# Performance work log

Measured on AMD Instinct MI355X. Metric: run time of the kernel, lower is better.

## Reference

```python
import jax, jax.numpy as jnp
import numpy as np

B, T, D, H = 4, 4096, 1024, 16
DH = D // H
NB = T // 2 + 1  # rfft bins


def setup_inputs() -> dict:
    key = jax.random.key(0)
    ks = jax.random.split(key, 6)
    x = jax.random.normal(ks[0], (B, T, D), dtype=jnp.float32)
    # torch nn.Linear params: weight [out, in], bias [out]
    W_qkv = jax.random.normal(ks[1], (3 * D, D), dtype=jnp.float32) * 0.02
    b_qkv = jnp.zeros((3 * D,), dtype=jnp.float32)
    W_o = jax.random.normal(ks[2], (D, D), dtype=jnp.float32) * 0.02
    b_o = jnp.zeros((D,), dtype=jnp.float32)
    # per-head per-bin spectral filters (smart-init-like small values)
    log_gain = jax.random.normal(ks[3], (H, NB), dtype=jnp.float32) * 0.05
    phase = jax.random.normal(ks[4], (H, NB), dtype=jnp.float32) * 0.01
    return {"x": x, "W_qkv": W_qkv, "b_qkv": b_qkv, "W_o": W_o,
            "b_o": b_o, "log_gain": log_gain, "phase": phase}


def reference(x, W_qkv, b_qkv, W_o, b_o, log_gain, phase):
    # qkv projection; only v is used on the spectral path (q,k discarded)
    qkv = jnp.einsum('btd,ed->bte', x, W_qkv) + b_qkv  # [B,T,3D]
    v = qkv[..., 2 * D:]                               # [B,T,D]
    v = v.reshape(B, T, H, DH).transpose(0, 2, 1, 3)   # [B,H,T,DH]
    # rFFT along the token dim
    v_f = jnp.fft.rfft(v.astype(jnp.float32), axis=2)  # [B,H,NB,DH] complex
    # per-head per-bin complex filter: polar(exp(log_gain), phase)
    mag = jnp.exp(log_gain)
    comp = jax.lax.complex(mag * jnp.cos(phase), mag * jnp.sin(phase))  # [H,NB]
    v_f = v_f * comp[None, :, :, None]
    y_h = jnp.fft.irfft(v_f, n=T, axis=2)              # [B,H,T,DH]
    y = y_h.transpose(0, 2, 1, 3).reshape(B, T, D)     # [B,T,D]
    y = jnp.einsum('btd,ed->bte', y, W_o) + b_o
    return x + y
```

## Files before the change

kernel.cpp:

```cpp
#include <hip/hip_runtime.h>
#include <hip/hip_bf16.h>
#include <math.h>

#define B_BATCH 4
#define T_LEN   4096
#define D_DIM   1024
#define H_HEADS 16
#define NB_BINS 2049
#define M_ROWS  (B_BATCH * T_LEN)

typedef __attribute__((ext_vector_type(8))) short short8;
typedef __attribute__((ext_vector_type(8))) unsigned short u16x8;
typedef __attribute__((ext_vector_type(4))) float f32x4;

__device__ __forceinline__ ushort f2bf(float f) {
    unsigned b = __float_as_uint(f);
    unsigned r = (b + 0x7fffu + ((b >> 16) & 1u)) >> 16;
    return (ushort)r;
}
__device__ __forceinline__ float bf2f(ushort u) {
    return __uint_as_float(((unsigned)u) << 16);
}
__device__ __forceinline__ u16x8 pack8(const float4& a, const float4& b) {
    u16x8 o;
    o[0] = f2bf(a.x); o[1] = f2bf(a.y); o[2] = f2bf(a.z); o[3] = f2bf(a.w);
    o[4] = f2bf(b.x); o[5] = f2bf(b.y); o[6] = f2bf(b.z); o[7] = f2bf(b.w);
    return o;
}

__global__ void cvt_weights(const float* __restrict__ wv, const float* __restrict__ wo,
                            ushort* __restrict__ wvb, ushort* __restrict__ wob, int n4) {
    int i = blockIdx.x * 256 + threadIdx.x;
    const float* src = (i < n4) ? wv : wo;
    ushort* dst = (i < n4) ? wvb : wob;
    int j = (i < n4) ? i : (i - n4);
    float4 v = ((const float4*)src)[j];
    ushort4 o;
    o.x = f2bf(v.x); o.y = f2bf(v.y); o.z = f2bf(v.z); o.w = f2bf(v.w);
    ((ushort4*)dst)[j] = o;
}

__device__ __forceinline__ int drev16(int i) {
    return ((i & 15) << 8) | (i & 0xF0) | (i >> 8);
}

__global__ void prep_tables(const float* __restrict__ lg, const float* __restrict__ ph,
                            float2* __restrict__ Cdr, float2* __restrict__ tw) {
    int idx = blockIdx.x * 256 + threadIdx.x;
    if (idx < 4096) {
        double th = -2.0 * 3.14159265358979323846 * (double)idx / 4096.0;
        tw[idx] = make_float2((float)cos(th), (float)sin(th));
    }
    if (idx >= H_HEADS * 4096) return;
    int h = idx >> 12, i = idx & 4095;
    int f = drev16(i);
    int fc = (f <= 2048) ? f : (4096 - f);
    float sgn = (f <= 2048) ? 1.f : -1.f;
    float m = expf(lg[h * NB_BINS + fc]) * (1.0f / 4096.0f);
    float p = ph[h * NB_BINS + fc];
    float re = m * __cosf(p), im = sgn * m * __sinf(p);
    if (fc == 0 || fc == 2048) im = 0.f;
    Cdr[idx] = make_float2(re, im);
}

template<bool RESID, bool BIASROW, bool BF32>
__global__ __launch_bounds__(512, 1) void gemm256(const ushort* __restrict__ A,
        const void* __restrict__ Bv, const float* __restrict__ bias,
        const float* __restrict__ resid, void* __restrict__ Cout,
        int M, int N, int K) {
    __shared__ ushort lds[65536];
    const int tid  = threadIdx.x;
    const int lane = tid & 63;
    const int wid  = tid >> 6;
    const int wr   = wid >> 2, wc = wid & 3;
    const int fr   = lane & 15;
    const int nbn  = N >> 8;
    int bid = (int)blockIdx.x;
    bid = (bid & 7) * ((int)gridDim.x >> 3) + (bid >> 3);
    int bm, bn;
    if (BF32) { const int nbm = M >> 8; bm = bid % nbm; bn = bid / nbm; }
    else      { bm = bid / nbn; bn = bid % nbn; }
    const int row0 = bm << 8, col0 = bn << 8;
    const int NT = K >> 6;

    const ushort* Bu = (const ushort*)Bv;
    const float*  Bf = (const float*)Bv;

    f32x4 acc[8][4];
#pragma unroll
    for (int i = 0; i < 8; i++)
#pragma unroll
        for (int j = 0; j < 4; j++) acc[i][j] = (f32x4){0.f, 0.f, 0.f, 0.f};

    auto stageA = [&](int t, int s) {
        int base = (((t & 1) << 1) + s) << 13;
        int k0 = (t << 6) + (s << 5);
#pragma unroll
        for (int i = 0; i < 2; i++) {
            int r = (wid << 5) + (i << 4) + (lane >> 2);
            int c = ((lane & 3) ^ ((lane >> 3) & 3)) << 3;
            const ushort* g = A + (size_t)(row0 + r) * (size_t)K + (size_t)(k0 + c);
            __builtin_amdgcn_global_load_lds(
                (const __attribute__((address_space(1))) void*)g,
                (__attribute__((address_space(3))) void*)&lds[base + (((wid << 1) + i) << 9)],
                16, 0, 0);
        }
    };
    auto stageB = [&](int t, int s) {
        int base = 32768 + ((((t & 1) << 1) + s) << 13);
        int k0 = (t << 6) + (s << 5);
#pragma unroll
        for (int i = 0; i < 2; i++) {
            int r = (wid << 5) + (i << 4) + (lane >> 2);
            int c = ((lane & 3) ^ ((lane >> 3) & 3)) << 3;
            const ushort* g = Bu + (size_t)(col0 + r) * (size_t)K + (size_t)(k0 + c);
            __builtin_amdgcn_global_load_lds(
                (const __attribute__((address_space(1))) void*)g,
                (__attribute__((address_space(3))) void*)&lds[base + (((wid << 1) + i) << 9)],
                16, 0, 0);
        }
    };
    auto issueB = [&](int t, int s, float4 bR[2][2]) {
#pragma unroll
        for (int i = 0; i < 2; i++) {
            int row = (wid << 5) + (i << 4) + (lane >> 2);
            int cc  = lane & 3;
            const float* g = Bf + (size_t)(col0 + row) * (size_t)K
                           + (size_t)((t << 6) + (s << 5) + (cc << 3));
            bR[i][0] = *(const float4*)g;
            bR[i][1] = *(const float4*)(g + 4);
        }
    };
    auto writeB = [&](int t, int s, float4 bR[2][2]) {
        int base = 32768 + ((((t & 1) << 1) + s) << 13);
#pragma unroll
        for (int i = 0; i < 2; i++) {
            int row = (wid << 5) + (i << 4) + (lane >> 2);
            int cc  = lane & 3;
            int slot = cc ^ ((row >> 1) & 3);
            *(u16x8*)&lds[base + (row << 5) + (slot << 3)] = pack8(bR[i][0], bR[i][1]);
        }
    };
    auto rdfrag = [&](int base, int row) -> short8 {
        int g = (((lane >> 4) ^ ((row >> 1) & 3)) << 3);
        return *(const short8*)&lds[base + (row << 5) + g];
    };

    stageA(0, 0); stageA(0, 1);
    if (BF32) {
        float4 bR0[2][2], bR1[2][2];
        issueB(0, 0, bR0); issueB(0, 1, bR1);
        writeB(0, 0, bR0); writeB(0, 1, bR1);
    } else {
        stageB(0, 0); stageB(0, 1);
    }
    __syncthreads();

    for (int t = 0; t < NT; ++t) {
        const int d = t & 1;
        const bool pre = (t + 1) < NT;
        float4 bR[2][2];
        if (pre) {
            stageA(t + 1, 0); stageA(t + 1, 1);
            if (BF32) issueB(t + 1, 0, bR);
            else { stageB(t + 1, 0); stageB(t + 1, 1); }
        }
        {
            const int ab = (((d << 1) + 0) << 13);
            const int bb = 32768 + (((d << 1) + 0) << 13);
            short8 bFr[4], aF[4];
#pragma unroll
            for (int ni = 0; ni < 4; ni++) bFr[ni] = rdfrag(bb, (wc << 6) + (ni << 4) + fr);
#pragma unroll
            for (int mh = 0; mh < 2; mh++) {
#pragma unroll
                for (int mi = 0; mi < 4; mi++)
                    aF[mi] = rdfrag(ab, (wr << 7) + (mh << 6) + (mi << 4) + fr);
#pragma unroll
                for (int mi = 0; mi < 4; mi++)
#pragma unroll
                    for (int ni = 0; ni < 4; ni++)
                        acc[(mh << 2) + mi][ni] = __builtin_amdgcn_mfma_f32_16x16x32_bf16(
                            aF[mi], bFr[ni], acc[(mh << 2) + mi][ni], 0, 0, 0);
            }
        }
        if (BF32 && pre) { writeB(t + 1, 0, bR); issueB(t + 1, 1, bR); }
        {
            const int ab = (((d << 1) + 1) << 13);
            const int bb = 32768 + (((d << 1) + 1) << 13);
            short8 bFr[4], aF[4];
#pragma unroll
            for (int ni = 0; ni < 4; ni++) bFr[ni] = rdfrag(bb, (wc << 6) + (ni << 4) + fr);
#pragma unroll
            for (int mh = 0; mh < 2; mh++) {
#pragma unroll
                for (int mi = 0; mi < 4; mi++)
                    aF[mi] = rdfrag(ab, (wr << 7) + (mh << 6) + (mi << 4) + fr);
#pragma unroll
                for (int mi = 0; mi < 4; mi++)
#pragma unroll
                    for (int ni = 0; ni < 4; ni++)
                        acc[(mh << 2) + mi][ni] = __builtin_amdgcn_mfma_f32_16x16x32_bf16(
                            aF[mi], bFr[ni], acc[(mh << 2) + mi][ni], 0, 0, 0);
            }
        }
        if (BF32 && pre) writeB(t + 1, 1, bR);
        __syncthreads();
    }

    const int crow = (lane >> 4) << 2;
#pragma unroll
    for (int mi = 0; mi < 8; mi++) {
#pragma unroll
        for (int ni = 0; ni < 4; ni++) {
            int row = row0 + (wr << 7) + (mi << 4) + crow;
            int col = col0 + (wc << 6) + (ni << 4) + fr;
            float bcol = BIASROW ? 0.f : bias[col];
#pragma unroll
            for (int j = 0; j < 4; j++) {
                float v = acc[mi][ni][j] + (BIASROW ? bias[row + j] : bcol);
                size_t off = (size_t)(row + j) * N + col;
                if (RESID) ((float*)Cout)[off] = resid[off] + v;
                else       ((ushort*)Cout)[off] = f2bf(v);
            }
        }
    }
}

__device__ __forceinline__ float2 cadd(float2 a, float2 b){ return make_float2(a.x+b.x, a.y+b.y); }
__device__ __forceinline__ float2 csub(float2 a, float2 b){ return make_float2(a.x-b.x, a.y-b.y); }
__device__ __forceinline__ float2 jmulp(float2 z){ return make_float2(-z.y, z.x); }
__device__ __forceinline__ float2 cmul(float2 a, float2 b){
    return make_float2(fmaf(a.x,b.x,-a.y*b.y), fmaf(a.x,b.y, a.y*b.x)); }
__device__ __forceinline__ float2 cmulc(float2 a, float2 b){
    return make_float2(fmaf(a.x,b.x, a.y*b.y), fmaf(a.y,b.x,-a.x*b.y)); }

template<int INV>
__device__ __forceinline__ void bf4(float2& a, float2& b, float2& c, float2& d) {
    float2 acp = cadd(a,c), acm = csub(a,c);
    float2 bdp = cadd(b,d), bdm = csub(b,d);
    float2 jb  = jmulp(bdm);
    a = cadd(acp, bdp);
    c = csub(acp, bdp);
    if (INV) { b = cadd(acm, jb); d = csub(acm, jb); }
    else     { b = csub(acm, jb); d = cadd(acm, jb); }
}

#define C16_1 0.9238795325112867f
#define S16_1 0.3826834323650898f
#define R16_2 0.7071067811865476f

template<int INV>
__device__ __forceinline__ void dft16(float2 v[16]) {
    const float sg = INV ? 1.f : -1.f;
    bf4<INV>(v[0], v[4], v[8],  v[12]);
    bf4<INV>(v[1], v[5], v[9],  v[13]);
    bf4<INV>(v[2], v[6], v[10], v[14]);
    bf4<INV>(v[3], v[7], v[11], v[15]);
    const float2 w1 = make_float2( C16_1, sg*S16_1);
    const float2 w2 = make_float2( R16_2, sg*R16_2);
    const float2 w3 = make_float2( S16_1, sg*C16_1);
    const float2 w6 = make_float2(-R16_2, sg*R16_2);
    const float2 w9 = make_float2(-C16_1,-sg*S16_1);
    v[5]  = cmul(v[5],  w1);
    v[6]  = cmul(v[6],  w2);
    v[7]  = cmul(v[7],  w3);
    v[9]  = cmul(v[9],  w2);
    v[10] = INV ? jmulp(v[10]) : make_float2(v[10].y, -v[10].x);
    v[11] = cmul(v[11], w6);
    v[13] = cmul(v[13], w3);
    v[14] = cmul(v[14], w6);
    v[15] = cmul(v[15], w9);
    bf4<INV>(v[0],  v[1],  v[2],  v[3]);
    bf4<INV>(v[4],  v[5],  v[6],  v[7]);
    bf4<INV>(v[8],  v[9],  v[10], v[11]);
    bf4<INV>(v[12], v[13], v[14], v[15]);
}

__host__ __device__ constexpr int oidx(int r) { return ((r & 3) << 2) | (r >> 2); }

template<int INV>
__device__ __forceinline__ void dft16p(float2 v[16]) {
    const float sg = INV ? 1.f : -1.f;
    bf4<INV>(v[oidx(0)], v[oidx(4)], v[oidx(8)],  v[oidx(12)]);
    bf4<INV>(v[oidx(1)], v[oidx(5)], v[oidx(9)],  v[oidx(13)]);
    bf4<INV>(v[oidx(2)], v[oidx(6)], v[oidx(10)], v[oidx(14)]);
    bf4<INV>(v[oidx(3)], v[oidx(7)], v[oidx(11)], v[oidx(15)]);
    const float2 w1 = make_float2( C16_1, sg*S16_1);
    const float2 w2 = make_float2( R16_2, sg*R16_2);
    const float2 w3 = make_float2( S16_1, sg*C16_1);
    const float2 w6 = make_float2(-R16_2, sg*R16_2);
    const float2 w9 = make_float2(-C16_1,-sg*S16_1);
    v[oidx(5)]  = cmul(v[oidx(5)],  w1);
    v[oidx(6)]  = cmul(v[oidx(6)],  w2);
    v[oidx(7)]  = cmul(v[oidx(7)],  w3);
    v[oidx(9)]  = cmul(v[oidx(9)],  w2);
    v[oidx(10)] = INV ? jmulp(v[oidx(10)]) : make_float2(v[oidx(10)].y, -v[oidx(10)].x);
    v[oidx(11)] = cmul(v[oidx(11)], w6);
    v[oidx(13)] = cmul(v[oidx(13)], w3);
    v[oidx(14)] = cmul(v[oidx(14)], w6);
    v[oidx(15)] = cmul(v[oidx(15)], w9);
    bf4<INV>(v[oidx(0)],  v[oidx(1)],  v[oidx(2)],  v[oidx(3)]);
    bf4<INV>(v[oidx(4)],  v[oidx(5)],  v[oidx(6)],  v[oidx(7)]);
    bf4<INV>(v[oidx(8)],  v[oidx(9)],  v[oidx(10)], v[oidx(11)]);
    bf4<INV>(v[oidx(12)], v[oidx(13)], v[oidx(14)], v[oidx(15)]);
}

__device__ __forceinline__ int phz(int t) { return t ^ (((t >> 4) ^ (t >> 8)) & 15); }

template<typename F>
__device__ __forceinline__ void tw_powers(float2 w1, F&& apply) {
    apply(1, w1);
    float2 w2 = cmul(w1, w1);   apply(2, w2);
    float2 w3 = cmul(w2, w1);   apply(3, w3);
    float2 w4 = cmul(w2, w2);   apply(4, w4);
    float2 w5 = cmul(w4, w1);   apply(5, w5);
    float2 w6 = cmul(w4, w2);   apply(6, w6);
    float2 w7 = cmul(w4, w3);   apply(7, w7);
    float2 w8 = cmul(w4, w4);   apply(8, w8);
    apply(9,  cmul(w8, w1));
    apply(10, cmul(w8, w2));
    apply(11, cmul(w8, w3));
    apply(12, cmul(w8, w4));
    apply(13, cmul(w8, w5));
    apply(14, cmul(w8, w6));
    apply(15, cmul(w8, w7));
}

__global__ __launch_bounds__(256) void fft16_filter(const ushort* __restrict__ VT,
                                                    ushort* __restrict__ yT,
                                                    const float2* __restrict__ tw,
                                                    const float2* __restrict__ Cdr) {
    __shared__ float2 X[2][4096];
    const int tid = threadIdx.x;
    const int b   = blockIdx.x >> 8;
    const int qb  = blockIdx.x & 255;
    const int d0  = qb << 2;
    const int h   = qb >> 4;

    float2 v[2][16];
#pragma unroll
    for (int p = 0; p < 2; p++) {
        const ushort* sRe = VT + (size_t)(d0 + 2 * p) * M_ROWS + b * T_LEN;
        const ushort* sIm = VT + (size_t)(d0 + 2 * p + 1) * M_ROWS + b * T_LEN;
#pragma unroll
        for (int j = 0; j < 16; j++)
            v[p][j] = make_float2(bf2f(sRe[tid + (j << 8)]), bf2f(sIm[tid + (j << 8)]));
    }

    dft16<0>(v[0]);
    dft16<0>(v[1]);
    {
        float2 w1 = tw[tid];
        tw_powers(w1, [&](int r, float2 w) {
            v[0][oidx(r)] = cmul(v[0][oidx(r)], w);
            v[1][oidx(r)] = cmul(v[1][oidx(r)], w);
        });
    }
#pragma unroll
    for (int r = 0; r < 16; r++) {
        int a = phz(tid + (r << 8));
        X[0][a] = v[0][oidx(r)];
        X[1][a] = v[1][oidx(r)];
    }
    __syncthreads();

    const int p2 = tid & 15, g2 = tid >> 4;
    const int base2 = (g2 << 8) + p2;
#pragma unroll
    for (int j = 0; j < 16; j++) {
        int a = phz(base2 + (j << 4));
        v[0][j] = X[0][a];
        v[1][j] = X[1][a];
    }
    dft16<0>(v[0]);
    dft16<0>(v[1]);
#pragma unroll
    for (int r = 1; r < 16; r++) {
        float2 w = tw[(p2 * r) << 4];
        v[0][oidx(r)] = cmul(v[0][oidx(r)], w);
        v[1][oidx(r)] = cmul(v[1][oidx(r)], w);
    }
#pragma unroll
    for (int r = 0; r < 16; r++) {
        int a = phz(base2 + (r << 4));
        X[0][a] = v[0][oidx(r)];
        X[1][a] = v[1][oidx(r)];
    }
    __syncthreads();

    const int base3 = tid << 4;
#pragma unroll
    for (int j = 0; j < 16; j++) {
        int a = phz(base3 + j);
        v[0][j] = X[0][a];
        v[1][j] = X[1][a];
    }
    dft16<0>(v[0]);
    dft16<0>(v[1]);
    const float2* Ch = Cdr + (h << 12) + base3;
#pragma unroll
    for (int r = 0; r < 16; r++) {
        float2 c = Ch[r];
        v[0][oidx(r)] = cmul(v[0][oidx(r)], c);
        v[1][oidx(r)] = cmul(v[1][oidx(r)], c);
    }
    dft16p<1>(v[0]);
    dft16p<1>(v[1]);
#pragma unroll
    for (int r = 0; r < 16; r++) {
        int a = phz(base3 + r);
        X[0][a] = v[0][r];
        X[1][a] = v[1][r];
    }
    __syncthreads();

#pragma unroll
    for (int j = 0; j < 16; j++) {
        int a = phz(base2 + (j << 4));
        v[0][j] = X[0][a];
        v[1][j] = X[1][a];
    }
#pragma unroll
    for (int j = 1; j < 16; j++) {
        float2 w = tw[(p2 * j) << 4];
        v[0][j] = cmulc(v[0][j], w);
        v[1][j] = cmulc(v[1][j], w);
    }
    dft16<1>(v[0]);
    dft16<1>(v[1]);
#pragma unroll
    for (int r = 0; r < 16; r++) {
        int a = phz(base2 + (r << 4));
        X[0][a] = v[0][oidx(r)];
        X[1][a] = v[1][oidx(r)];
    }
    __syncthreads();

#pragma unroll
    for (int j = 0; j < 16; j++) {
        int a = phz(tid + (j << 8));
        v[0][j] = X[0][a];
        v[1][j] = X[1][a];
    }
    {
        float2 w1 = tw[tid];
        tw_powers(w1, [&](int r, float2 w) {
            v[0][r] = cmulc(v[0][r], w);
            v[1][r] = cmulc(v[1][r], w);
        });
    }
    dft16<1>(v[0]);
    dft16<1>(v[1]);
#pragma unroll
    for (int p = 0; p < 2; p++) {
        ushort* dRe = yT + (size_t)(d0 + 2 * p) * M_ROWS + b * T_LEN;
        ushort* dIm = yT + (size_t)(d0 + 2 * p + 1) * M_ROWS + b * T_LEN;
#pragma unroll
        for (int r = 0; r < 16; r++) {
            float2 val = v[p][oidx(r)];
            dRe[tid + (r << 8)] = f2bf(val.x);
            dIm[tid + (r << 8)] = f2bf(val.y);
        }
    }
}

__global__ __launch_bounds__(256) void transpose_yT(const ushort* __restrict__ src,
                                                    ushort* __restrict__ dst) {
    __shared__ ushort tile[4096];
    const int tid = threadIdx.x;
    const int bm = blockIdx.x & 255;
    const int bd = blockIdx.x >> 8;
    const int m0 = bm << 6, d0 = bd << 6;
#pragma unroll
    for (int i = 0; i < 2; i++) {
        int vn = tid + (i << 8);
        int r  = vn >> 3;
        int c8 = (vn & 7) << 3;
        u16x8 val = *(const u16x8*)&src[(size_t)(d0 + r) * M_ROWS + m0 + c8];
#pragma unroll
        for (int q = 0; q < 8; q++)
            tile[(r << 6) | ((c8 + q) ^ r)] = (ushort)val[q];
    }
    __syncthreads();
    const int dc = tid & 63;
    const int wb = tid >> 6;
#pragma unroll
    for (int i = 0; i < 16; i++) {
        int mr = wb + (i << 2);
        dst[(size_t)(m0 + mr) * D_DIM + d0 + dc] = tile[(dc << 6) | (mr ^ dc)];
    }
}

extern "C" void kernel_launch(void* const* d_in, const int* in_sizes, int n_in,
                              void* d_out, int out_size, void* d_ws, size_t ws_size,
                              hipStream_t stream) {
    const float* x    = (const float*)d_in[0];
    const float* Wqkv = (const float*)d_in[1];
    const float* bqkv = (const float*)d_in[2];
    const float* Wo   = (const float*)d_in[3];
    const float* bo   = (const float*)d_in[4];
    const float* lg   = (const float*)d_in[5];
    const float* ph   = (const float*)d_in[6];

    char* ws = (char*)d_ws;
    ushort* ynat = (ushort*)ws;
    ushort* Wvb = (ushort*)(ws + 33554432);
    ushort* Wob = (ushort*)(ws + 35651584);
    float2* tw  = (float2*)(ws + 37748736);
    float2* Cdr = (float2*)(ws + 37781504);

    ushort* VT   = (ushort*)d_out;
    ushort* yT   = (ushort*)((char*)d_out + 33554432);
    float*  out  = (float*)d_out;

    prep_tables<<<(H_HEADS * 4096) / 256, 256, 0, stream>>>(lg, ph, Cdr, tw);
    cvt_weights<<<2 * (1048576 / 4) / 256, 256, 0, stream>>>(
        Wqkv + 2048 * 1024, Wo, Wvb, Wob, 1048576 / 4);

    gemm256<false, true, true><<<(D_DIM / 256) * (M_ROWS / 256), 512, 0, stream>>>(
        Wvb, (const void*)x, bqkv + 2 * D_DIM, nullptr, (void*)VT, D_DIM, M_ROWS, D_DIM);

    fft16_filter<<<B_BATCH * (D_DIM / 4), 256, 0, stream>>>(VT, yT, tw, Cdr);

    transpose_yT<<<(M_ROWS / 64) * (D_DIM / 64), 256, 0, stream>>>(yT, ynat);

    gemm256<true, false, false><<<(M_ROWS / 256) * (D_DIM / 256), 512, 0, stream>>>(
        ynat, (const void*)Wob, bo, x, (void*)out, M_ROWS, D_DIM, D_DIM);
}
```

Before: 150.2 us.

## Fuse yT transpose into output GEMM A-tile loading

Removes the separate transpose kernel. The output GEMM now reads the d-major yT buffer directly, loading through registers and scattering into the swizzled LDS layout. This saves a full 32 MB read and write pass plus one launch. The cost is that the A operand no longer uses async global_load_lds, and the transposed LDS writes are 16 scalar ushort stores per thread, which may add LDS bank conflicts and register pressure.

```diff
diff --git a/kernel.cpp b/kernel.cpp
--- a/kernel.cpp
+++ b/kernel.cpp
@@ -63,7 +63,7 @@
     Cdr[idx] = make_float2(re, im);
 }
 
-template<bool RESID, bool BIASROW, bool BF32>
+template<bool RESID, bool BIASROW, bool BF32, bool ATR>
 __global__ __launch_bounds__(512, 1) void gemm256(const ushort* __restrict__ A,
         const void* __restrict__ Bv, const float* __restrict__ bias,
         const float* __restrict__ resid, void* __restrict__ Cout,
@@ -106,6 +106,30 @@
                 16, 0, 0);
         }
     };
+    auto issueA_tr = [&](int t, int s, u16x8 aR[2]) {
+        int dl = tid & 31;
+        int m0 = (tid >> 5) << 4;
+        const ushort* g = A + (size_t)((t << 6) + (s << 5) + dl) * (size_t)M
+                        + (size_t)(row0 + m0);
+        aR[0] = *(const u16x8*)g;
+        aR[1] = *(const u16x8*)(g + 8);
+    };
+    auto writeA_tr = [&](int t, int s, u16x8 aR[2]) {
+        int base = (((t & 1) << 1) + s) << 13;
+        int dl = tid & 31;
+        int m0 = (tid >> 5) << 4;
+        int ch = dl >> 3, d7 = dl & 7;
+#pragma unroll
+        for (int j = 0; j < 8; j++) {
+            int m = m0 + j;
+            lds[base + (m << 5) + ((ch ^ ((m >> 1) & 3)) << 3) + d7] = aR[0][j];
+        }
+#pragma unroll
+        for (int j = 0; j < 8; j++) {
+            int m = m0 + 8 + j;
+            lds[base + (m << 5) + ((ch ^ ((m >> 1) & 3)) << 3) + d7] = aR[1][j];
+        }
+    };
     auto stageB = [&](int t, int s) {
         int base = 32768 + ((((t & 1) << 1) + s) << 13);
         int k0 = (t << 6) + (s << 5);
@@ -146,7 +170,13 @@
         return *(const short8*)&lds[base + (row << 5) + g];
     };
 
-    stageA(0, 0); stageA(0, 1);
+    if (ATR) {
+        u16x8 aR0[2], aR1[2];
+        issueA_tr(0, 0, aR0); issueA_tr(0, 1, aR1);
+        writeA_tr(0, 0, aR0); writeA_tr(0, 1, aR1);
+    } else {
+        stageA(0, 0); stageA(0, 1);
+    }
     if (BF32) {
         float4 bR0[2][2], bR1[2][2];
         issueB(0, 0, bR0); issueB(0, 1, bR1);
@@ -160,8 +190,10 @@
         const int d = t & 1;
         const bool pre = (t + 1) < NT;
         float4 bR[2][2];
+        u16x8 aR[2];
         if (pre) {
-            stageA(t + 1, 0); stageA(t + 1, 1);
+            if (ATR) issueA_tr(t + 1, 0, aR);
+            else { stageA(t + 1, 0); stageA(t + 1, 1); }
             if (BF32) issueB(t + 1, 0, bR);
             else { stageB(t + 1, 0); stageB(t + 1, 1); }
         }
@@ -184,7 +216,10 @@
                             aF[mi], bFr[ni], acc[(mh << 2) + mi][ni], 0, 0, 0);
             }
         }
-        if (BF32 && pre) { writeB(t + 1, 0, bR); issueB(t + 1, 1, bR); }
+        if (pre) {
+            if (ATR) { writeA_tr(t + 1, 0, aR); issueA_tr(t + 1, 1, aR); }
+            if (BF32) { writeB(t + 1, 0, bR); issueB(t + 1, 1, bR); }
+        }
         {
             const int ab = (((d << 1) + 1) << 13);
             const int bb = 32768 + (((d << 1) + 1) << 13);
@@ -204,7 +239,10 @@
                             aF[mi], bFr[ni], acc[(mh << 2) + mi][ni], 0, 0, 0);
             }
         }
-        if (BF32 && pre) writeB(t + 1, 1, bR);
+        if (pre) {
+            if (ATR) writeA_tr(t + 1, 1, aR);
+            if (BF32) writeB(t + 1, 1, bR);
+        }
         __syncthreads();
     }
 
@@ -465,33 +503,6 @@
     }
 }
 
-__global__ __launch_bounds__(256) void transpose_yT(const ushort* __restrict__ src,
-                                                    ushort* __restrict__ dst) {
-    __shared__ ushort tile[4096];
-    const int tid = threadIdx.x;
-    const int bm = blockIdx.x & 255;
-    const int bd = blockIdx.x >> 8;
-    const int m0 = bm << 6, d0 = bd << 6;
-#pragma unroll
-    for (int i = 0; i < 2; i++) {
-        int vn = tid + (i << 8);
-        int r  = vn >> 3;
-        int c8 = (vn & 7) << 3;
-        u16x8 val = *(const u16x8*)&src[(size_t)(d0 + r) * M_ROWS + m0 + c8];
-#pragma unroll
-        for (int q = 0; q < 8; q++)
-            tile[(r << 6) | ((c8 + q) ^ r)] = (ushort)val[q];
-    }
-    __syncthreads();
-    const int dc = tid & 63;
-    const int wb = tid >> 6;
-#pragma unroll
-    for (int i = 0; i < 16; i++) {
-        int mr = wb + (i << 2);
-        dst[(size_t)(m0 + mr) * D_DIM + d0 + dc] = tile[(dc << 6) | (mr ^ dc)];
-    }
-}
-
 extern "C" void kernel_launch(void* const* d_in, const int* in_sizes, int n_in,
                               void* d_out, int out_size, void* d_ws, size_t ws_size,
                               hipStream_t stream) {
@@ -504,27 +515,24 @@
     const float* ph   = (const float*)d_in[6];
 
     char* ws = (char*)d_ws;
-    ushort* ynat = (ushort*)ws;
+    ushort* yT  = (ushort*)ws;
     ushort* Wvb = (ushort*)(ws + 33554432);
     ushort* Wob = (ushort*)(ws + 35651584);
     float2* tw  = (float2*)(ws + 37748736);
     float2* Cdr = (float2*)(ws + 37781504);
 
-    ushort* VT   = (ushort*)d_out;
-    ushort* yT   = (ushort*)((char*)d_out + 33554432);
-    float*  out  = (float*)d_out;
+    ushort* VT  = (ushort*)d_out;
+    float*  out = (float*)d_out;
 
     prep_tables<<<(H_HEADS * 4096) / 256, 256, 0, stream>>>(lg, ph, Cdr, tw);
     cvt_weights<<<2 * (1048576 / 4) / 256, 256, 0, stream>>>(
         Wqkv + 2048 * 1024, Wo, Wvb, Wob, 1048576 / 4);
 
-    gemm256<false, true, true><<<(D_DIM / 256) * (M_ROWS / 256), 512, 0, stream>>>(
+    gemm256<false, true, true, false><<<(D_DIM / 256) * (M_ROWS / 256), 512, 0, stream>>>(
         Wvb, (const void*)x, bqkv + 2 * D_DIM, nullptr, (void*)VT, D_DIM, M_ROWS, D_DIM);
 
     fft16_filter<<<B_BATCH * (D_DIM / 4), 256, 0, stream>>>(VT, yT, tw, Cdr);
 
-    transpose_yT<<<(M_ROWS / 64) * (D_DIM / 64), 256, 0, stream>>>(yT, ynat);
-
-    gemm256<true, false, false><<<(M_ROWS / 256) * (D_DIM / 256), 512, 0, stream>>>(
-        ynat, (const void*)Wob, bo, x, (void*)out, M_ROWS, D_DIM, D_DIM);
-}
+    gemm256<true, false, false, true><<<(M_ROWS / 256) * (D_DIM / 256), 512, 0, stream>>>(
+        yT, (const void*)Wob, bo, x, (void*)out, M_ROWS, D_DIM, D_DIM);
+}
```

Result: faster. 144.4 us (median of 2 runs) (-3.9%).
